# Kernel tuning notes

Measured on AMD Instinct MI355X. Metric: run time of the kernel, lower is better.

Reference implementation:

```python
import jax, jax.numpy as jnp
import numpy as np
import math

NQ = 8          # qubits
DIM = 2 ** NQ   # 256-dim state vector
NVL = 4         # variational layers
EPS = 1e-5      # LayerNorm eps (torch default)


def _ln(x, g, b):
    m = jnp.mean(x, -1, keepdims=True)
    v = jnp.mean((x - m) ** 2, -1, keepdims=True)
    return (x - m) / jnp.sqrt(v + EPS) * g + b


def _apply_ry(state, q, theta):
    # state: (B, 256); qubit q is the 2**q 'pre' axis (PennyLane wire 0 = MSB)
    pre, post = 2 ** q, 2 ** (NQ - 1 - q)
    s = state.reshape(-1, pre, 2, post)
    c = jnp.cos(theta * 0.5)
    sn = jnp.sin(theta * 0.5)
    if jnp.ndim(theta) == 1:  # per-sample angle (input encoding)
        c = c[:, None, None]
        sn = sn[:, None, None]
    a0 = s[:, :, 0, :]
    a1 = s[:, :, 1, :]
    return jnp.stack([c * a0 - sn * a1, sn * a0 + c * a1], axis=2).reshape(state.shape)


def _apply_cnot(state, ctrl):
    # CNOT with control=ctrl, target=ctrl+1 (adjacent wires)
    pre = 2 ** ctrl
    s = state.reshape(-1, pre, 2, 2, 2 ** (NQ - 2 - ctrl))
    new = jnp.stack([s[:, :, 0], s[:, :, 1, ::-1]], axis=2)
    return new.reshape(state.shape)


def _vqc(inputs, weights):
    # inputs: (B, 8), weights: (4, 8) -> (B, 8) PauliZ expectations
    B = inputs.shape[0]
    # Hadamard layer on |0...0> -> uniform real superposition, amp = 1/16
    state = jnp.full((B, DIM), 1.0 / 16.0, dtype=inputs.dtype)
    for q in range(NQ):
        state = _apply_ry(state, q, inputs[:, q])
    for l in range(NVL):
        for c in range(0, NQ - 1, 2):
            state = _apply_cnot(state, c)
        for c in range(1, NQ - 1, 2):
            state = _apply_cnot(state, c)
        for q in range(NQ):
            state = _apply_ry(state, q, weights[l, q])
    p = state * state  # state stays real (H, RY, CNOT are real gates)
    zs = []
    for q in range(NQ):
        pr = p.reshape(B, 2 ** q, 2, 2 ** (NQ - 1 - q))
        zs.append(pr[:, :, 0, :].sum((1, 2)) - pr[:, :, 1, :].sum((1, 2)))
    return jnp.stack(zs, axis=1)


def reference(x, pe, emb_w, emb_b, emb_g, emb_bt, ip_w, ip_b, in_g, in_b,
              wq_i, wq_f, wq_g, wq_o, pi_w, pi_b, pf_w, pf_b, pg_w, pg_b,
              po_w, po_b, on_g, on_b, out_w, out_b):
    B, T, _ = x.shape
    H = emb_w.shape[0]
    # embedding + LayerNorm (dropout = identity in eval) + positional encoding
    emb = _ln(x @ emb_w.T + emb_b, emb_g, emb_bt) + pe[None, :T]

    def step(carry, x_t):
        h, c = carry
        comb = jnp.concatenate([x_t, h], axis=1)
        proj = _ln(jnp.tanh(comb @ ip_w.T + ip_b), in_g, in_b)
        i_t = jax.nn.sigmoid(_vqc(proj, wq_i) @ pi_w.T + pi_b)
        f_t = jax.nn.sigmoid(_vqc(proj, wq_f) @ pf_w.T + pf_b)
        g_t = jnp.tanh(_vqc(proj, wq_g) @ pg_w.T + pg_b)
        o_t = jax.nn.sigmoid(_vqc(proj, wq_o) @ po_w.T + po_b)
        c_n = f_t * c + i_t * g_t
        h_n = o_t * jnp.tanh(c_n)
        out_t = _ln(h_n + x_t, on_g, on_b)
        return (h_n, c_n), out_t

    h0 = jnp.zeros((B, H), x.dtype)
    xs = jnp.swapaxes(emb, 0, 1)  # (T, B, H)
    _, outs = jax.lax.scan(jax.checkpoint(step), (h0, h0), xs)
    out = jnp.swapaxes(outs, 0, 1)  # (B, T, H)
    return out @ out_w.T + out_b


def setup_inputs() -> dict:
    B, T, IN, H, OUT = 1024, 128, 8, 128, 1
    key = jax.random.key(0)
    ks = jax.random.split(key, 12)

    def kaiming_u(k, shape, fan_in):
        bnd = math.sqrt(6.0 / fan_in)
        return jax.random.uniform(k, shape, jnp.float32, -bnd, bnd)

    # sinusoidal positional encoding
    pe = np.zeros((T, H), np.float32)
    pos = np.arange(T, dtype=np.float32)[:, None]
    div = np.exp(np.arange(0, H, 2, dtype=np.float32) * (-math.log(10000.0) / H))
    pe[:, 0::2] = np.sin(pos * div)
    pe[:, 1::2] = np.cos(pos * div)

    return {
        'x': jax.random.normal(ks[0], (B, T, IN), jnp.float32),
        'pe': jnp.asarray(pe),
        'emb_w': kaiming_u(ks[1], (H, IN), IN), 'emb_b': jnp.zeros((H,), jnp.float32),
        'emb_g': jnp.ones((H,), jnp.float32), 'emb_bt': jnp.zeros((H,), jnp.float32),
        'ip_w': kaiming_u(ks[2], (NQ, 2 * H), 2 * H), 'ip_b': jnp.zeros((NQ,), jnp.float32),
        'in_g': jnp.ones((NQ,), jnp.float32), 'in_b': jnp.zeros((NQ,), jnp.float32),
        'wq_i': 0.01 * jax.random.normal(ks[3], (NVL, NQ), jnp.float32),
        'wq_f': 0.01 * jax.random.normal(ks[4], (NVL, NQ), jnp.float32),
        'wq_g': 0.01 * jax.random.normal(ks[5], (NVL, NQ), jnp.float32),
        'wq_o': 0.01 * jax.random.normal(ks[6], (NVL, NQ), jnp.float32),
        'pi_w': kaiming_u(ks[7], (H, NQ), NQ), 'pi_b': jnp.zeros((H,), jnp.float32),
        'pf_w': kaiming_u(ks[8], (H, NQ), NQ), 'pf_b': jnp.zeros((H,), jnp.float32),
        'pg_w': kaiming_u(ks[9], (H, NQ), NQ), 'pg_b': jnp.zeros((H,), jnp.float32),
        'po_w': kaiming_u(ks[10], (H, NQ), NQ), 'po_b': jnp.zeros((H,), jnp.float32),
        'on_g': jnp.ones((H,), jnp.float32), 'on_b': jnp.zeros((H,), jnp.float32),
        'out_w': kaiming_u(ks[11], (OUT, H), H), 'out_b': jnp.zeros((OUT,), jnp.float32),
    }
```

## Files before the change

kernel.cpp:

```cpp
#include <hip/hip_runtime.h>

#define Tv 128

typedef float v2 __attribute__((ext_vector_type(2)));

__device__ __forceinline__ v2 pkfma(v2 a, v2 b, v2 c) {
  return __builtin_elementwise_fma(a, b, c);
}

template<int CTRL>
__device__ __forceinline__ float dppx(float x) {
  return __int_as_float(__builtin_amdgcn_update_dpp(0, __float_as_int(x), CTRL, 0xF, 0xF, true));
}
__device__ __forceinline__ float dpp_rm(float x, int ctrl, int rm) {
  switch (ctrl) {
    default: return 0.f;
    case 0x111: return __int_as_float(__builtin_amdgcn_update_dpp(0, __float_as_int(x), 0x111, 0xF, 0xF, true));
    case 0x112: return __int_as_float(__builtin_amdgcn_update_dpp(0, __float_as_int(x), 0x112, 0xF, 0xF, true));
    case 0x114: return __int_as_float(__builtin_amdgcn_update_dpp(0, __float_as_int(x), 0x114, 0xF, 0xF, true));
    case 0x118: return __int_as_float(__builtin_amdgcn_update_dpp(0, __float_as_int(x), 0x118, 0xF, 0xF, true));
    case 0x142: return __int_as_float(__builtin_amdgcn_update_dpp(0, __float_as_int(x), 0x142, 0xA, 0xF, true));
    case 0x143: return __int_as_float(__builtin_amdgcn_update_dpp(0, __float_as_int(x), 0x143, 0xC, 0xF, true));
  }
}
__device__ __forceinline__ float wave_sum(float x) {
  x += dpp_rm(x, 0x111, 0xF);
  x += dpp_rm(x, 0x112, 0xF);
  x += dpp_rm(x, 0x114, 0xF);
  x += dpp_rm(x, 0x118, 0xF);
  x += dpp_rm(x, 0x142, 0xA);
  x += dpp_rm(x, 0x143, 0xC);
  return __int_as_float(__builtin_amdgcn_readlane(__float_as_int(x), 63));
}
template<int M>
__device__ __forceinline__ float lane_xor(float x) {
  if constexpr (M == 1)       return dppx<0xB1>(x);
  else if constexpr (M == 2)  return dppx<0x4E>(x);
  else if constexpr (M == 8)  return dppx<0x128>(x);
  else if constexpr (M == 32) return __shfl_xor(x, 32, 64);
  else return __int_as_float(__builtin_amdgcn_ds_swizzle(__float_as_int(x), (M << 10) | 0x1F));
}
__device__ __forceinline__ float bperm(int addr, float x) {
  return __int_as_float(__builtin_amdgcn_ds_bpermute(addr, __float_as_int(x)));
}
__device__ __forceinline__ float rdlane(float x, int l) {
  return __int_as_float(__builtin_amdgcn_readlane(__float_as_int(x), l));
}
__device__ __forceinline__ float fast_rcp(float x){ return __builtin_amdgcn_rcpf(x); }
__device__ __forceinline__ float fast_rsq(float x){ return __builtin_amdgcn_rsqf(x); }
__device__ __forceinline__ float tanh_(float x){
  float e = __expf(2.0f * x);
  return 1.0f - 2.0f * fast_rcp(e + 1.0f);
}
__device__ __forceinline__ float sigm_(float x){
  return fast_rcp(1.0f + __expf(-x));
}

__device__ __forceinline__ float transpose_reduce8(const v2* P2, int L) {
  const int bb0 = L & 1, bb1 = L & 2, bb2 = L & 4;
  float q_[4];
  #pragma unroll
  for (int k = 0; k < 4; k++) {
    float keep = bb0 ? P2[k].y : P2[k].x;
    float send = bb0 ? P2[k].x : P2[k].y;
    q_[k] = keep + lane_xor<1>(send);
  }
  float r_[2];
  #pragma unroll
  for (int k = 0; k < 2; k++) {
    float keep = bb1 ? q_[2 * k + 1] : q_[2 * k];
    float send = bb1 ? q_[2 * k]     : q_[2 * k + 1];
    r_[k] = keep + lane_xor<2>(send);
  }
  float u;
  {
    float keep = bb2 ? r_[1] : r_[0];
    float send = bb2 ? r_[0] : r_[1];
    u = keep + lane_xor<4>(send);
  }
  u += lane_xor<8>(u); u += lane_xor<16>(u); u += lane_xor<32>(u);
  return u;
}

template<int M>
__device__ __forceinline__ void ry_lane_t(v2* S, float ts) {
  v2 ts2 = {ts, ts};
  #pragma unroll
  for (int k = 0; k < 4; k++) {
    v2 o;
    o.x = lane_xor<M>(S[k].x);
    o.y = lane_xor<M>(S[k].y);
    S[k] = pkfma(ts2, o, S[k]);
  }
}


struct __align__(16) SMem {
  float tt[4][36];
  float ipb[8][4];
  float zbuf[32];
  float embp[2][2];
  float projp[2][8];
  float outp[2][4];
};

__global__ __launch_bounds__(128, 2) void qlstm_kernel(
    const float* __restrict__ x,     const float* __restrict__ pe,
    const float* __restrict__ emb_w, const float* __restrict__ emb_b,
    const float* __restrict__ emb_g, const float* __restrict__ emb_bt,
    const float* __restrict__ ip_w,  const float* __restrict__ ip_b,
    const float* __restrict__ in_g,  const float* __restrict__ in_b,
    const float* __restrict__ wq_i,  const float* __restrict__ wq_f,
    const float* __restrict__ wq_gt, const float* __restrict__ wq_o,
    const float* __restrict__ pi_w,  const float* __restrict__ pi_b,
    const float* __restrict__ pf_w,  const float* __restrict__ pf_b,
    const float* __restrict__ pg_w,  const float* __restrict__ pg_b,
    const float* __restrict__ po_w,  const float* __restrict__ po_b,
    const float* __restrict__ on_g,  const float* __restrict__ on_b,
    const float* __restrict__ out_w, const float* __restrict__ out_b,
    float* __restrict__ out)
{
  __shared__ SMem sm;
  const int tid = threadIdx.x;
  const int b   = blockIdx.x;
  const int w   = tid >> 6;
  const int L   = tid & 63;
  const int l5  = L & 31;
  const int gate = w * 2 + (L >> 5);
  const int o8  = L & 7;

  {
    int gg = tid >> 5, rem = tid & 31;
    const float* wsel = (gg == 0) ? wq_i : (gg == 1) ? wq_f : (gg == 2) ? wq_gt : wq_o;
    float th = wsel[rem] * 0.5f;
    float cc = __cosf(th), ss = __sinf(th);
    sm.tt[gg][rem] = ss * fast_rcp(cc);
    float v = cc;
    v *= lane_xor<1>(v); v *= lane_xor<2>(v); v *= lane_xor<4>(v);
    v *= lane_xor<8>(v); v *= lane_xor<16>(v);
    if (rem == 0) sm.tt[gg][32] = v * v;
  }
  if (tid < 8) {
    sm.ipb[tid][0] = ip_b[tid];
    sm.ipb[tid][1] = in_g[tid];
    sm.ipb[tid][2] = in_b[tid];
    sm.ipb[tid][3] = 0.0f;
  }

  const int j = tid;
  v2 EW[4];
  {
    float4 a = *reinterpret_cast<const float4*>(emb_w + j * 8);
    float4 c = *reinterpret_cast<const float4*>(emb_w + j * 8 + 4);
    EW[0] = {a.x, a.y}; EW[1] = {a.z, a.w}; EW[2] = {c.x, c.y}; EW[3] = {c.z, c.w};
  }
  float ebb = emb_b[j], egg = emb_g[j], ebt = emb_bt[j];
  v2 IPW1[4], IPW2[4];
  #pragma unroll
  for (int k = 0; k < 4; k++) {
    IPW1[k] = {ip_w[(2 * k) * 256 + j],       ip_w[(2 * k + 1) * 256 + j]};
    IPW2[k] = {ip_w[(2 * k) * 256 + 128 + j], ip_w[(2 * k + 1) * 256 + 128 + j]};
  }
  v2 GW[4][4];
  #pragma unroll
  for (int gg = 0; gg < 4; gg++) {
    const float* pw = (gg == 0) ? pi_w : (gg == 1) ? pf_w : (gg == 2) ? pg_w : po_w;
    float4 a = *reinterpret_cast<const float4*>(pw + j * 8);
    float4 c = *reinterpret_cast<const float4*>(pw + j * 8 + 4);
    GW[gg][0] = {a.x, a.y}; GW[gg][1] = {a.z, a.w};
    GW[gg][2] = {c.x, c.y}; GW[gg][3] = {c.z, c.w};
  }
  float gb[4] = {pi_b[j], pf_b[j], pg_b[j], po_b[j]};
  float ong = on_g[j], onb = on_b[j], ow_ = out_w[j];
  float outb = out_b[0];
  float a_ = ong * ow_;

  const int grp = L & 32;
  int aC0, aC1;
  {
    int l1 = l5 ^ ((l5 & 16) >> 1) ^ ((l5 & 4) >> 1);
    int lb = l1 ^ ((l1 & 8) >> 1) ^ ((l1 & 2) >> 1);
    aC0 = (grp | lb) << 2;
    aC1 = (grp | (lb ^ 16)) << 2;
  }

  float h = 0.f, c = 0.f;
  const float* xbase = x + (size_t)b * Tv * 8;

  {
    float uw = transpose_reduce8(EW, L);
    float eb1 = wave_sum(ebb);
    if (L < 8) sm.projp[w][L] = uw;
    if (L == 0) sm.embp[w][0] = eb1;
  }
  __syncthreads();

  v2 WB[4]; float bS;
  {
    #pragma unroll
    for (int k = 0; k < 4; k++) {
      WB[k].x = (sm.projp[0][2 * k]     + sm.projp[1][2 * k])     * 0.0078125f;
      WB[k].y = (sm.projp[0][2 * k + 1] + sm.projp[1][2 * k + 1]) * 0.0078125f;
    }
    bS = (sm.embp[0][0] + sm.embp[1][0]) * 0.0078125f;
  }
  float4 ipbv = *reinterpret_cast<float4*>(&sm.ipb[o8][0]);
  v2 LT0[4], LT1[4], LNTS[4];
  float LTS[4][5];
  float ct2g = sm.tt[gate][32];
  {
    const float* tg = sm.tt[gate];
    #pragma unroll
    for (int l = 0; l < 4; l++) {
      float4 qa = *reinterpret_cast<const float4*>(tg + l * 8);
      float4 qb = *reinterpret_cast<const float4*>(tg + l * 8 + 4);
      LT0[l]  = {qa.x, qa.x};
      LT1[l]  = {qa.y, qa.y};
      LNTS[l] = {-qa.z, qa.z};
      float tq[5] = {qa.w, qb.x, qb.y, qb.z, qb.w};
      #pragma unroll
      for (int q = 0; q < 5; q++) {
        int m = 16 >> q;
        LTS[l][q] = (l5 & m) ? tq[q] : -tq[q];
      }
    }
  }

  float e;
  {
    float4 a = *reinterpret_cast<const float4*>(xbase);
    float4 cq = *reinterpret_cast<const float4*>(xbase + 4);
    v2 XT[4] = {{a.x,a.y},{a.z,a.w},{cq.x,cq.y},{cq.z,cq.w}};
    v2 acc = XT[0] * EW[0];
    acc = pkfma(XT[1], EW[1], acc);
    acc = pkfma(XT[2], EW[2], acc);
    acc = pkfma(XT[3], EW[3], acc);
    float er = ebb + acc.x + acc.y;
    float s2 = wave_sum(er * er);
    float r0 = wave_sum(a_), r1 = wave_sum(onb * ow_);
    if (L == 0) {
      sm.embp[w][1] = s2;
      sm.outp[w][0] = r0; sm.outp[w][1] = r1;
    }
    __syncthreads();
    v2 mac = XT[0] * WB[0];
    mac = pkfma(XT[1], WB[1], mac);
    mac = pkfma(XT[2], WB[2], mac);
    mac = pkfma(XT[3], WB[3], mac);
    float mn = mac.x + mac.y + bS;
    float s2t = sm.embp[0][1] + sm.embp[1][1];
    float vr = fmaf(s2t, 0.0078125f, -mn * mn);
    float inv = fast_rsq(vr + 1e-5f);
    e = (er - mn) * inv * egg + ebt + pe[j];
  }
  const float SW = sm.outp[0][0] + sm.outp[1][0];
  const float KB = sm.outp[0][1] + sm.outp[1][1] + outb;

  #pragma unroll 1
  for (int t = 0; t < Tv; t++) {
    v2 XN[4]; float pen;
    {
      int tn = (t + 1) & (Tv - 1);
      float4 a = *reinterpret_cast<const float4*>(xbase + tn * 8);
      float4 cq = *reinterpret_cast<const float4*>(xbase + tn * 8 + 4);
      XN[0] = {a.x,a.y}; XN[1] = {a.z,a.w}; XN[2] = {cq.x,cq.y}; XN[3] = {cq.z,cq.w};
      pen = pe[tn * 128 + j];
    }

    const v2 e2 = {e, e}, h2 = {h, h};
    v2 P2[4];
    #pragma unroll
    for (int k = 0; k < 4; k++)
      P2[k] = pkfma(e2, IPW1[k], h2 * IPW2[k]);
    float u = transpose_reduce8(P2, L);
    if (L < 8) sm.projp[w][L] = u;
    __syncthreads();
    u += sm.projp[1 - w][o8];
    if (t && tid == 0) {
      float sy  = sm.outp[0][0] + sm.outp[1][0];
      float sy2 = sm.outp[0][1] + sm.outp[1][1];
      float sya = sm.outp[0][2] + sm.outp[1][2];
      float mn2 = sy * 0.0078125f;
      float vr2 = fmaf(sy2, 0.0078125f, -mn2 * mn2);
      float inv2 = fast_rsq(vr2 + 1e-5f);
      out[b * Tv + t - 1] = fmaf(inv2, sya - mn2 * SW, KB);
    }

    float tv = tanh_(u + ipbv.x);
    float m1 = tv, m2 = tv * tv;
    m1 += lane_xor<1>(m1); m2 += lane_xor<1>(m2);
    m1 += lane_xor<2>(m1); m2 += lane_xor<2>(m2);
    m1 += lane_xor<4>(m1); m2 += lane_xor<4>(m2);
    float pm = m1 * 0.125f;
    float pv = fmaf(m2, 0.125f, -pm * pm);
    float theta = (tv - pm) * fast_rsq(pv + 1e-5f) * ipbv.y + ipbv.z;
    float ph = theta * 0.5f;
    float cE = __cosf(ph), sE = __sinf(ph);
    float fm = cE - sE, fp = cE + sE;
    float f_[16];
    #pragma unroll
    for (int qq = 0; qq < 8; qq++) {
      f_[2 * qq]     = rdlane(fm, qq);
      f_[2 * qq + 1] = rdlane(fp, qq);
    }

    v2 S[4];
    {
      float g01_[4];
      #pragma unroll
      for (int i = 0; i < 4; i++)
        g01_[i] = f_[(i >> 1) & 1] * f_[2 + (i & 1)];
      float lf = f_[6 + ((l5 >> 4) & 1)] * f_[8 + ((l5 >> 3) & 1)]
               * f_[10 + ((l5 >> 2) & 1)] * f_[12 + ((l5 >> 1) & 1)]
               * f_[14 + (l5 & 1)];
      lf *= 0.0625f;
      const v2 F45 = {f_[4], f_[5]};
      #pragma unroll
      for (int k = 0; k < 4; k++) {
        float tk = lf * g01_[k];
        v2 tk2 = {tk, tk};
        S[k] = tk2 * F45;
      }
    }

    #pragma unroll
    for (int l = 0; l < 4; l++) {
      v2 N0, N1, N2, N3;
      N0.x = bperm(aC0, S[0].x); N0.y = bperm(aC1, S[0].y);
      N1.x = bperm(aC1, S[1].y); N1.y = bperm(aC0, S[1].x);
      N2.x = bperm(aC0, S[3].x); N2.y = bperm(aC1, S[3].y);
      N3.x = bperm(aC1, S[2].y); N3.y = bperm(aC0, S[2].x);
      S[0] = N0; S[1] = N1; S[2] = N2; S[3] = N3;
      {
        v2 t0 = LT0[l];
        v2 a0 = S[0], a1 = S[1];
        S[0] = pkfma(-t0, S[2], S[0]);
        S[2] = pkfma( t0, a0,  S[2]);
        S[1] = pkfma(-t0, S[3], S[1]);
        S[3] = pkfma( t0, a1,  S[3]);
      }
      {
        v2 t1 = LT1[l];
        v2 a0 = S[0], a2 = S[2];
        S[0] = pkfma(-t1, S[1], S[0]);
        S[1] = pkfma( t1, a0,  S[1]);
        S[2] = pkfma(-t1, S[3], S[2]);
        S[3] = pkfma( t1, a2,  S[3]);
      }
      {
        v2 nts = LNTS[l];
        #pragma unroll
        for (int k = 0; k < 4; k++) {
          v2 aa = S[k];
          v2 sw = __builtin_shufflevector(aa, aa, 1, 0);
          S[k] = pkfma(nts, sw, aa);
        }
      }
      ry_lane_t<16>(S, LTS[l][0]);
      ry_lane_t<8>(S, LTS[l][1]);
      ry_lane_t<4>(S, LTS[l][2]);
      ry_lane_t<2>(S, LTS[l][3]);
      ry_lane_t<1>(S, LTS[l][4]);
    }

    v2 P[4];
    #pragma unroll
    for (int k = 0; k < 4; k++) P[k] = S[k] * S[k];
    v2 A = P[0] + P[2];
    v2 B = P[1] + P[3];
    v2 D = (P[0] - P[2]) + (P[1] - P[3]);
    float z0 = D.x + D.y;
    v2 Ev = A - B;
    float z1 = Ev.x + Ev.y;
    v2 G = A + B;
    float z2 = G.x - G.y;
    float S_ = G.x + G.y;
    z0 += lane_xor<1>(z0); z1 += lane_xor<1>(z1); z2 += lane_xor<1>(z2);
    z0 += lane_xor<2>(z0); z1 += lane_xor<2>(z1); z2 += lane_xor<2>(z2);
    z0 += lane_xor<4>(z0); z1 += lane_xor<4>(z1); z2 += lane_xor<4>(z2);
    z0 += lane_xor<8>(z0); z1 += lane_xor<8>(z1); z2 += lane_xor<8>(z2);
    z0 += lane_xor<16>(z0); z1 += lane_xor<16>(z1); z2 += lane_xor<16>(z2);
    float v, d, uS;
    v = lane_xor<16>(S_); d = S_ - v; uS = S_ + v;
    float z3 = (l5 & 16) ? -d : d;
    z3 += lane_xor<8>(z3); z3 += lane_xor<4>(z3); z3 += lane_xor<2>(z3); z3 += lane_xor<1>(z3);
    v = lane_xor<8>(uS); d = uS - v; uS = uS + v;
    float z4 = (l5 & 8) ? -d : d;
    z4 += lane_xor<4>(z4); z4 += lane_xor<2>(z4); z4 += lane_xor<1>(z4);
    v = lane_xor<4>(uS); d = uS - v; uS = uS + v;
    float z5 = (l5 & 4) ? -d : d;
    z5 += lane_xor<2>(z5); z5 += lane_xor<1>(z5);
    v = lane_xor<2>(uS); d = uS - v; uS = uS + v;
    float z6 = (l5 & 2) ? -d : d;
    z6 += lane_xor<1>(z6);
    v = lane_xor<1>(uS); d = uS - v;
    float z7 = (l5 & 1) ? -d : d;

    if (l5 < 8) {
      float zv = z0;
      zv = (l5 == 1) ? z1 : zv;
      zv = (l5 == 2) ? z2 : zv;
      zv = (l5 == 3) ? z3 : zv;
      zv = (l5 == 4) ? z4 : zv;
      zv = (l5 == 5) ? z5 : zv;
      zv = (l5 == 6) ? z6 : zv;
      zv = (l5 == 7) ? z7 : zv;
      sm.zbuf[gate * 8 + l5] = zv * ct2g;
    }

    v2 acc = XN[0] * EW[0];
    acc = pkfma(XN[1], EW[1], acc);
    acc = pkfma(XN[2], EW[2], acc);
    acc = pkfma(XN[3], EW[3], acc);
    float en_raw = ebb + acc.x + acc.y;
    {
      float s2n = wave_sum(en_raw * en_raw);
      if (L == 0) sm.embp[w][0] = s2n;
    }
    __syncthreads();

    float acg[4];
    #pragma unroll
    for (int gg = 0; gg < 4; gg++) {
      float4 za0 = *reinterpret_cast<float4*>(&sm.zbuf[gg * 8]);
      float4 za1 = *reinterpret_cast<float4*>(&sm.zbuf[gg * 8 + 4]);
      v2 Z0 = {za0.x, za0.y}, Z1 = {za0.z, za0.w};
      v2 Z2 = {za1.x, za1.y}, Z3 = {za1.z, za1.w};
      v2 av = Z0 * GW[gg][0];
      av = pkfma(Z1, GW[gg][1], av);
      av = pkfma(Z2, GW[gg][2], av);
      av = pkfma(Z3, GW[gg][3], av);
      acg[gg] = gb[gg] + av.x + av.y;
    }
    float it = sigm_(acg[0]), ft = sigm_(acg[1]), gt = tanh_(acg[2]), ot = sigm_(acg[3]);
    c = ft * c + it * gt;
    h = ot * tanh_(c);

    float en;
    {
      float s2 = sm.embp[0][0] + sm.embp[1][0];
      v2 mac = XN[0] * WB[0];
      mac = pkfma(XN[1], WB[1], mac);
      mac = pkfma(XN[2], WB[2], mac);
      mac = pkfma(XN[3], WB[3], mac);
      float mn = mac.x + mac.y + bS;
      float vr = fmaf(s2, 0.0078125f, -mn * mn);
      float inv = fast_rsq(vr + 1e-5f);
      en = (en_raw - mn) * inv * egg + ebt + pen;
    }

    {
      float y = h + e;
      float ry0 = wave_sum(y), ry1 = wave_sum(y * y), ry2 = wave_sum(y * a_);
      if (L == 0) { sm.outp[w][0] = ry0; sm.outp[w][1] = ry1; sm.outp[w][2] = ry2; }
    }
    e = en;
  }

  __syncthreads();
  if (tid == 0) {
    float sy  = sm.outp[0][0] + sm.outp[1][0];
    float sy2 = sm.outp[0][1] + sm.outp[1][1];
    float sya = sm.outp[0][2] + sm.outp[1][2];
    float mn2 = sy * 0.0078125f;
    float vr2 = fmaf(sy2, 0.0078125f, -mn2 * mn2);
    float inv2 = fast_rsq(vr2 + 1e-5f);
    out[b * Tv + Tv - 1] = fmaf(inv2, sya - mn2 * SW, KB);
  }
}

extern "C" void kernel_launch(void* const* d_in, const int* in_sizes, int n_in,
                              void* d_out, int out_size, void* d_ws, size_t ws_size,
                              hipStream_t stream) {
  qlstm_kernel<<<dim3(1024), dim3(128), 0, stream>>>(
      (const float*)d_in[0],  (const float*)d_in[1],  (const float*)d_in[2],  (const float*)d_in[3],
      (const float*)d_in[4],  (const float*)d_in[5],  (const float*)d_in[6],  (const float*)d_in[7],
      (const float*)d_in[8],  (const float*)d_in[9],  (const float*)d_in[10], (const float*)d_in[11],
      (const float*)d_in[12], (const float*)d_in[13], (const float*)d_in[14], (const float*)d_in[15],
      (const float*)d_in[16], (const float*)d_in[17], (const float*)d_in[18], (const float*)d_in[19],
      (const float*)d_in[20], (const float*)d_in[21], (const float*)d_in[22], (const float*)d_in[23],
      (const float*)d_in[24], (const float*)d_in[25],
      (float*)d_out);
}
```

Baseline: 549.7 us.

## Process two batch sequences per block to interleave independent recurrences

Each block now runs two independent batch elements (b and b+512) through the recurrent loop together, halving the grid to 512 blocks. Work for both sequences is interleaved between the same barriers, so the per-step __syncthreads and shuffle latency is shared and there is more independent work to hide latency. The cost is higher register pressure: launch bounds drop to one block per SIMD group, so occupancy may fall and spilling is possible.

```diff
diff --git a/kernel.cpp b/kernel.cpp
--- a/kernel.cpp
+++ b/kernel.cpp
@@ -1,6 +1,7 @@
 #include <hip/hip_runtime.h>
 
 #define Tv 128
+#define BH 512
 
 typedef float v2 __attribute__((ext_vector_type(2)));
 
@@ -98,13 +99,13 @@
 struct __align__(16) SMem {
   float tt[4][36];
   float ipb[8][4];
-  float zbuf[32];
-  float embp[2][2];
-  float projp[2][8];
-  float outp[2][4];
+  float zbuf[2][32];
+  float embp[2][2][2];
+  float projp[2][2][8];
+  float outp[2][2][4];
 };
 
-__global__ __launch_bounds__(128, 2) void qlstm_kernel(
+__global__ __launch_bounds__(128, 1) void qlstm_kernel(
     const float* __restrict__ x,     const float* __restrict__ pe,
     const float* __restrict__ emb_w, const float* __restrict__ emb_b,
     const float* __restrict__ emb_g, const float* __restrict__ emb_bt,
@@ -184,14 +185,14 @@
     aC1 = (grp | (lb ^ 16)) << 2;
   }
 
-  float h = 0.f, c = 0.f;
-  const float* xbase = x + (size_t)b * Tv * 8;
+  float h[2] = {0.f, 0.f}, c[2] = {0.f, 0.f};
+  const float* xb[2] = { x + (size_t)b * Tv * 8, x + (size_t)(b + BH) * Tv * 8 };
 
   {
     float uw = transpose_reduce8(EW, L);
     float eb1 = wave_sum(ebb);
-    if (L < 8) sm.projp[w][L] = uw;
-    if (L == 0) sm.embp[w][0] = eb1;
+    if (L < 8) sm.projp[0][w][L] = uw;
+    if (L == 0) sm.embp[0][w][0] = eb1;
   }
   __syncthreads();
 
@@ -199,10 +200,10 @@
   {
     #pragma unroll
     for (int k = 0; k < 4; k++) {
-      WB[k].x = (sm.projp[0][2 * k]     + sm.projp[1][2 * k])     * 0.0078125f;
-      WB[k].y = (sm.projp[0][2 * k + 1] + sm.projp[1][2 * k + 1]) * 0.0078125f;
-    }
-    bS = (sm.embp[0][0] + sm.embp[1][0]) * 0.0078125f;
+      WB[k].x = (sm.projp[0][0][2 * k]     + sm.projp[0][1][2 * k])     * 0.0078125f;
+      WB[k].y = (sm.projp[0][0][2 * k + 1] + sm.projp[0][1][2 * k + 1]) * 0.0078125f;
+    }
+    bS = (sm.embp[0][0][0] + sm.embp[0][1][0]) * 0.0078125f;
   }
   float4 ipbv = *reinterpret_cast<float4*>(&sm.ipb[o8][0]);
   v2 LT0[4], LT1[4], LNTS[4];
@@ -226,86 +227,104 @@
     }
   }
 
-  float e;
-  {
-    float4 a = *reinterpret_cast<const float4*>(xbase);
-    float4 cq = *reinterpret_cast<const float4*>(xbase + 4);
-    v2 XT[4] = {{a.x,a.y},{a.z,a.w},{cq.x,cq.y},{cq.z,cq.w}};
-    v2 acc = XT[0] * EW[0];
-    acc = pkfma(XT[1], EW[1], acc);
-    acc = pkfma(XT[2], EW[2], acc);
-    acc = pkfma(XT[3], EW[3], acc);
-    float er = ebb + acc.x + acc.y;
-    float s2 = wave_sum(er * er);
+  float e[2];
+  {
+    v2 XT[2][4]; float er[2];
+    #pragma unroll
+    for (int ee = 0; ee < 2; ee++) {
+      float4 a = *reinterpret_cast<const float4*>(xb[ee]);
+      float4 cq = *reinterpret_cast<const float4*>(xb[ee] + 4);
+      XT[ee][0] = {a.x,a.y}; XT[ee][1] = {a.z,a.w};
+      XT[ee][2] = {cq.x,cq.y}; XT[ee][3] = {cq.z,cq.w};
+      v2 acc = XT[ee][0] * EW[0];
+      acc = pkfma(XT[ee][1], EW[1], acc);
+      acc = pkfma(XT[ee][2], EW[2], acc);
+      acc = pkfma(XT[ee][3], EW[3], acc);
+      er[ee] = ebb + acc.x + acc.y;
+      float s2 = wave_sum(er[ee] * er[ee]);
+      if (L == 0) sm.embp[ee][w][1] = s2;
+    }
     float r0 = wave_sum(a_), r1 = wave_sum(onb * ow_);
-    if (L == 0) {
-      sm.embp[w][1] = s2;
-      sm.outp[w][0] = r0; sm.outp[w][1] = r1;
-    }
+    if (L == 0) { sm.outp[0][w][0] = r0; sm.outp[0][w][1] = r1; }
     __syncthreads();
-    v2 mac = XT[0] * WB[0];
-    mac = pkfma(XT[1], WB[1], mac);
-    mac = pkfma(XT[2], WB[2], mac);
-    mac = pkfma(XT[3], WB[3], mac);
-    float mn = mac.x + mac.y + bS;
-    float s2t = sm.embp[0][1] + sm.embp[1][1];
-    float vr = fmaf(s2t, 0.0078125f, -mn * mn);
-    float inv = fast_rsq(vr + 1e-5f);
-    e = (er - mn) * inv * egg + ebt + pe[j];
-  }
-  const float SW = sm.outp[0][0] + sm.outp[1][0];
-  const float KB = sm.outp[0][1] + sm.outp[1][1] + outb;
+    #pragma unroll
+    for (int ee = 0; ee < 2; ee++) {
+      v2 mac = XT[ee][0] * WB[0];
+      mac = pkfma(XT[ee][1], WB[1], mac);
+      mac = pkfma(XT[ee][2], WB[2], mac);
+      mac = pkfma(XT[ee][3], WB[3], mac);
+      float mn = mac.x + mac.y + bS;
+      float s2t = sm.embp[ee][0][1] + sm.embp[ee][1][1];
+      float vr = fmaf(s2t, 0.0078125f, -mn * mn);
+      float inv = fast_rsq(vr + 1e-5f);
+      e[ee] = (er[ee] - mn) * inv * egg + ebt + pe[j];
+    }
+  }
+  const float SW = sm.outp[0][0][0] + sm.outp[0][1][0];
+  const float KB = sm.outp[0][0][1] + sm.outp[0][1][1] + outb;
 
   #pragma unroll 1
   for (int t = 0; t < Tv; t++) {
-    v2 XN[4]; float pen;
+    v2 XN[2][4]; float pen;
     {
       int tn = (t + 1) & (Tv - 1);
-      float4 a = *reinterpret_cast<const float4*>(xbase + tn * 8);
-      float4 cq = *reinterpret_cast<const float4*>(xbase + tn * 8 + 4);
-      XN[0] = {a.x,a.y}; XN[1] = {a.z,a.w}; XN[2] = {cq.x,cq.y}; XN[3] = {cq.z,cq.w};
+      #pragma unroll
+      for (int ee = 0; ee < 2; ee++) {
+        float4 a = *reinterpret_cast<const float4*>(xb[ee] + tn * 8);
+        float4 cq = *reinterpret_cast<const float4*>(xb[ee] + tn * 8 + 4);
+        XN[ee][0] = {a.x,a.y}; XN[ee][1] = {a.z,a.w};
+        XN[ee][2] = {cq.x,cq.y}; XN[ee][3] = {cq.z,cq.w};
+      }
       pen = pe[tn * 128 + j];
     }
 
-    const v2 e2 = {e, e}, h2 = {h, h};
-    v2 P2[4];
-    #pragma unroll
-    for (int k = 0; k < 4; k++)
-      P2[k] = pkfma(e2, IPW1[k], h2 * IPW2[k]);
-    float u = transpose_reduce8(P2, L);
-    if (L < 8) sm.projp[w][L] = u;
+    float u[2];
+    #pragma unroll
+    for (int ee = 0; ee < 2; ee++) {
+      const v2 e2 = {e[ee], e[ee]}, h2 = {h[ee], h[ee]};
+      v2 P2[4];
+      #pragma unroll
+      for (int k = 0; k < 4; k++)
+        P2[k] = pkfma(e2, IPW1[k], h2 * IPW2[k]);
+      u[ee] = transpose_reduce8(P2, L);
+      if (L < 8) sm.projp[ee][w][L] = u[ee];
+    }
     __syncthreads();
-    u += sm.projp[1 - w][o8];
+    u[0] += sm.projp[0][1 - w][o8];
+    u[1] += sm.projp[1][1 - w][o8];
     if (t && tid == 0) {
-      float sy  = sm.outp[0][0] + sm.outp[1][0];
-      float sy2 = sm.outp[0][1] + sm.outp[1][1];
-      float sya = sm.outp[0][2] + sm.outp[1][2];
-      float mn2 = sy * 0.0078125f;
-      float vr2 = fmaf(sy2, 0.0078125f, -mn2 * mn2);
-      float inv2 = fast_rsq(vr2 + 1e-5f);
-      out[b * Tv + t - 1] = fmaf(inv2, sya - mn2 * SW, KB);
-    }
-
-    float tv = tanh_(u + ipbv.x);
-    float m1 = tv, m2 = tv * tv;
-    m1 += lane_xor<1>(m1); m2 += lane_xor<1>(m2);
-    m1 += lane_xor<2>(m1); m2 += lane_xor<2>(m2);
-    m1 += lane_xor<4>(m1); m2 += lane_xor<4>(m2);
-    float pm = m1 * 0.125f;
-    float pv = fmaf(m2, 0.125f, -pm * pm);
-    float theta = (tv - pm) * fast_rsq(pv + 1e-5f) * ipbv.y + ipbv.z;
-    float ph = theta * 0.5f;
-    float cE = __cosf(ph), sE = __sinf(ph);
-    float fm = cE - sE, fp = cE + sE;
-    float f_[16];
-    #pragma unroll
-    for (int qq = 0; qq < 8; qq++) {
-      f_[2 * qq]     = rdlane(fm, qq);
-      f_[2 * qq + 1] = rdlane(fp, qq);
-    }
-
-    v2 S[4];
-    {
+      #pragma unroll
+      for (int ee = 0; ee < 2; ee++) {
+        float sy  = sm.outp[ee][0][0] + sm.outp[ee][1][0];
+        float sy2 = sm.outp[ee][0][1] + sm.outp[ee][1][1];
+        float sya = sm.outp[ee][0][2] + sm.outp[ee][1][2];
+        float mn2 = sy * 0.0078125f;
+        float vr2 = fmaf(sy2, 0.0078125f, -mn2 * mn2);
+        float inv2 = fast_rsq(vr2 + 1e-5f);
+        out[(size_t)(b + ee * BH) * Tv + t - 1] = fmaf(inv2, sya - mn2 * SW, KB);
+      }
+    }
+
+    v2 S[2][4];
+    #pragma unroll
+    for (int ee = 0; ee < 2; ee++) {
+      float tv = tanh_(u[ee] + ipbv.x);
+      float m1 = tv, m2 = tv * tv;
+      m1 += lane_xor<1>(m1); m2 += lane_xor<1>(m2);
+      m1 += lane_xor<2>(m1); m2 += lane_xor<2>(m2);
+      m1 += lane_xor<4>(m1); m2 += lane_xor<4>(m2);
+      float pm = m1 * 0.125f;
+      float pv = fmaf(m2, 0.125f, -pm * pm);
+      float theta = (tv - pm) * fast_rsq(pv + 1e-5f) * ipbv.y + ipbv.z;
+      float ph = theta * 0.5f;
+      float cE = __cosf(ph), sE = __sinf(ph);
+      float fm = cE - sE, fp = cE + sE;
+      float f_[16];
+      #pragma unroll
+      for (int qq = 0; qq < 8; qq++) {
+        f_[2 * qq]     = rdlane(fm, qq);
+        f_[2 * qq + 1] = rdlane(fp, qq);
+      }
       float g01_[4];
       #pragma unroll
       for (int i = 0; i < 4; i++)
@@ -319,160 +338,172 @@
       for (int k = 0; k < 4; k++) {
         float tk = lf * g01_[k];
         v2 tk2 = {tk, tk};
-        S[k] = tk2 * F45;
+        S[ee][k] = tk2 * F45;
       }
     }
 
     #pragma unroll
     for (int l = 0; l < 4; l++) {
-      v2 N0, N1, N2, N3;
-      N0.x = bperm(aC0, S[0].x); N0.y = bperm(aC1, S[0].y);
-      N1.x = bperm(aC1, S[1].y); N1.y = bperm(aC0, S[1].x);
-      N2.x = bperm(aC0, S[3].x); N2.y = bperm(aC1, S[3].y);
-      N3.x = bperm(aC1, S[2].y); N3.y = bperm(aC0, S[2].x);
-      S[0] = N0; S[1] = N1; S[2] = N2; S[3] = N3;
-      {
-        v2 t0 = LT0[l];
-        v2 a0 = S[0], a1 = S[1];
-        S[0] = pkfma(-t0, S[2], S[0]);
-        S[2] = pkfma( t0, a0,  S[2]);
-        S[1] = pkfma(-t0, S[3], S[1]);
-        S[3] = pkfma( t0, a1,  S[3]);
-      }
-      {
-        v2 t1 = LT1[l];
-        v2 a0 = S[0], a2 = S[2];
-        S[0] = pkfma(-t1, S[1], S[0]);
-        S[1] = pkfma( t1, a0,  S[1]);
-        S[2] = pkfma(-t1, S[3], S[2]);
-        S[3] = pkfma( t1, a2,  S[3]);
-      }
-      {
-        v2 nts = LNTS[l];
-        #pragma unroll
-        for (int k = 0; k < 4; k++) {
-          v2 aa = S[k];
-          v2 sw = __builtin_shufflevector(aa, aa, 1, 0);
-          S[k] = pkfma(nts, sw, aa);
+      #pragma unroll
+      for (int ee = 0; ee < 2; ee++) {
+        v2* Se = S[ee];
+        v2 N0, N1, N2, N3;
+        N0.x = bperm(aC0, Se[0].x); N0.y = bperm(aC1, Se[0].y);
+        N1.x = bperm(aC1, Se[1].y); N1.y = bperm(aC0, Se[1].x);
+        N2.x = bperm(aC0, Se[3].x); N2.y = bperm(aC1, Se[3].y);
+        N3.x = bperm(aC1, Se[2].y); N3.y = bperm(aC0, Se[2].x);
+        Se[0] = N0; Se[1] = N1; Se[2] = N2; Se[3] = N3;
+        {
+          v2 t0 = LT0[l];
+          v2 a0 = Se[0], a1 = Se[1];
+          Se[0] = pkfma(-t0, Se[2], Se[0]);
+          Se[2] = pkfma( t0, a0,  Se[2]);
+          Se[1] = pkfma(-t0, Se[3], Se[1]);
+          Se[3] = pkfma( t0, a1,  Se[3]);
         }
-      }
-      ry_lane_t<16>(S, LTS[l][0]);
-      ry_lane_t<8>(S, LTS[l][1]);
-      ry_lane_t<4>(S, LTS[l][2]);
-      ry_lane_t<2>(S, LTS[l][3]);
-      ry_lane_t<1>(S, LTS[l][4]);
-    }
-
-    v2 P[4];
-    #pragma unroll
-    for (int k = 0; k < 4; k++) P[k] = S[k] * S[k];
-    v2 A = P[0] + P[2];
-    v2 B = P[1] + P[3];
-    v2 D = (P[0] - P[2]) + (P[1] - P[3]);
-    float z0 = D.x + D.y;
-    v2 Ev = A - B;
-    float z1 = Ev.x + Ev.y;
-    v2 G = A + B;
-    float z2 = G.x - G.y;
-    float S_ = G.x + G.y;
-    z0 += lane_xor<1>(z0); z1 += lane_xor<1>(z1); z2 += lane_xor<1>(z2);
-    z0 += lane_xor<2>(z0); z1 += lane_xor<2>(z1); z2 += lane_xor<2>(z2);
-    z0 += lane_xor<4>(z0); z1 += lane_xor<4>(z1); z2 += lane_xor<4>(z2);
-    z0 += lane_xor<8>(z0); z1 += lane_xor<8>(z1); z2 += lane_xor<8>(z2);
-    z0 += lane_xor<16>(z0); z1 += lane_xor<16>(z1); z2 += lane_xor<16>(z2);
-    float v, d, uS;
-    v = lane_xor<16>(S_); d = S_ - v; uS = S_ + v;
-    float z3 = (l5 & 16) ? -d : d;
-    z3 += lane_xor<8>(z3); z3 += lane_xor<4>(z3); z3 += lane_xor<2>(z3); z3 += lane_xor<1>(z3);
-    v = lane_xor<8>(uS); d = uS - v; uS = uS + v;
-    float z4 = (l5 & 8) ? -d : d;
-    z4 += lane_xor<4>(z4); z4 += lane_xor<2>(z4); z4 += lane_xor<1>(z4);
-    v = lane_xor<4>(uS); d = uS - v; uS = uS + v;
-    float z5 = (l5 & 4) ? -d : d;
-    z5 += lane_xor<2>(z5); z5 += lane_xor<1>(z5);
-    v = lane_xor<2>(uS); d = uS - v; uS = uS + v;
-    float z6 = (l5 & 2) ? -d : d;
-    z6 += lane_xor<1>(z6);
-    v = lane_xor<1>(uS); d = uS - v;
-    float z7 = (l5 & 1) ? -d : d;
-
-    if (l5 < 8) {
-      float zv = z0;
-      zv = (l5 == 1) ? z1 : zv;
-      zv = (l5 == 2) ? z2 : zv;
-      zv = (l5 == 3) ? z3 : zv;
-      zv = (l5 == 4) ? z4 : zv;
-      zv = (l5 == 5) ? z5 : zv;
-      zv = (l5 == 6) ? z6 : zv;
-      zv = (l5 == 7) ? z7 : zv;
-      sm.zbuf[gate * 8 + l5] = zv * ct2g;
-    }
-
-    v2 acc = XN[0] * EW[0];
-    acc = pkfma(XN[1], EW[1], acc);
-    acc = pkfma(XN[2], EW[2], acc);
-    acc = pkfma(XN[3], EW[3], acc);
-    float en_raw = ebb + acc.x + acc.y;
-    {
-      float s2n = wave_sum(en_raw * en_raw);
-      if (L == 0) sm.embp[w][0] = s2n;
+        {
+          v2 t1 = LT1[l];
+          v2 a0 = Se[0], a2 = Se[2];
+          Se[0] = pkfma(-t1, Se[1], Se[0]);
+          Se[1] = pkfma( t1, a0,  Se[1]);
+          Se[2] = pkfma(-t1, Se[3], Se[2]);
+          Se[3] = pkfma( t1, a2,  Se[3]);
+        }
+        {
+          v2 nts = LNTS[l];
+          #pragma unroll
+          for (int k = 0; k < 4; k++) {
+            v2 aa = Se[k];
+            v2 sw = __builtin_shufflevector(aa, aa, 1, 0);
+            Se[k] = pkfma(nts, sw, aa);
+          }
+        }
+        ry_lane_t<16>(Se, LTS[l][0]);
+        ry_lane_t<8>(Se, LTS[l][1]);
+        ry_lane_t<4>(Se, LTS[l][2]);
+        ry_lane_t<2>(Se, LTS[l][3]);
+        ry_lane_t<1>(Se, LTS[l][4]);
+      }
+    }
+
+    #pragma unroll
+    for (int ee = 0; ee < 2; ee++) {
+      v2 P[4];
+      #pragma unroll
+      for (int k = 0; k < 4; k++) P[k] = S[ee][k] * S[ee][k];
+      v2 A = P[0] + P[2];
+      v2 B = P[1] + P[3];
+      v2 D = (P[0] - P[2]) + (P[1] - P[3]);
+      float z0 = D.x + D.y;
+      v2 Ev = A - B;
+      float z1 = Ev.x + Ev.y;
+      v2 G = A + B;
+      float z2 = G.x - G.y;
+      float S_ = G.x + G.y;
+      z0 += lane_xor<1>(z0); z1 += lane_xor<1>(z1); z2 += lane_xor<1>(z2);
+      z0 += lane_xor<2>(z0); z1 += lane_xor<2>(z1); z2 += lane_xor<2>(z2);
+      z0 += lane_xor<4>(z0); z1 += lane_xor<4>(z1); z2 += lane_xor<4>(z2);
+      z0 += lane_xor<8>(z0); z1 += lane_xor<8>(z1); z2 += lane_xor<8>(z2);
+      z0 += lane_xor<16>(z0); z1 += lane_xor<16>(z1); z2 += lane_xor<16>(z2);
+      float v, d, uS;
+      v = lane_xor<16>(S_); d = S_ - v; uS = S_ + v;
+      float z3 = (l5 & 16) ? -d : d;
+      z3 += lane_xor<8>(z3); z3 += lane_xor<4>(z3); z3 += lane_xor<2>(z3); z3 += lane_xor<1>(z3);
+      v = lane_xor<8>(uS); d = uS - v; uS = uS + v;
+      float z4 = (l5 & 8) ? -d : d;
+      z4 += lane_xor<4>(z4); z4 += lane_xor<2>(z4); z4 += lane_xor<1>(z4);
+      v = lane_xor<4>(uS); d = uS - v; uS = uS + v;
+      float z5 = (l5 & 4) ? -d : d;
+      z5 += lane_xor<2>(z5); z5 += lane_xor<1>(z5);
+      v = lane_xor<2>(uS); d = uS - v; uS = uS + v;
+      float z6 = (l5 & 2) ? -d : d;
+      z6 += lane_xor<1>(z6);
+      v = lane_xor<1>(uS); d = uS - v;
+      float z7 = (l5 & 1) ? -d : d;
+
+      if (l5 < 8) {
+        float zv = z0;
+        zv = (l5 == 1) ? z1 : zv;
+        zv = (l5 == 2) ? z2 : zv;
+        zv = (l5 == 3) ? z3 : zv;
+        zv = (l5 == 4) ? z4 : zv;
+        zv = (l5 == 5) ? z5 : zv;
+        zv = (l5 == 6) ? z6 : zv;
+        zv = (l5 == 7) ? z7 : zv;
+        sm.zbuf[ee][gate * 8 + l5] = zv * ct2g;
+      }
+    }
+
+    float en_raw[2];
+    #pragma unroll
+    for (int ee = 0; ee < 2; ee++) {
+      v2 acc = XN[ee][0] * EW[0];
+      acc = pkfma(XN[ee][1], EW[1], acc);
+      acc = pkfma(XN[ee][2], EW[2], acc);
+      acc = pkfma(XN[ee][3], EW[3], acc);
+      en_raw[ee] = ebb + acc.x + acc.y;
+      float s2n = wave_sum(en_raw[ee] * en_raw[ee]);
+      if (L == 0) sm.embp[ee][w][0] = s2n;
     }
     __syncthreads();
 
-    float acg[4];
-    #pragma unroll
-    for (int gg = 0; gg < 4; gg++) {
-      float4 za0 = *reinterpret_cast<float4*>(&sm.zbuf[gg * 8]);
-      float4 za1 = *reinterpret_cast<float4*>(&sm.zbuf[gg * 8 + 4]);
-      v2 Z0 = {za0.x, za0.y}, Z1 = {za0.z, za0.w};
-      v2 Z2 = {za1.x, za1.y}, Z3 = {za1.z, za1.w};
-      v2 av = Z0 * GW[gg][0];
-      av = pkfma(Z1, GW[gg][1], av);
-      av = pkfma(Z2, GW[gg][2], av);
-      av = pkfma(Z3, GW[gg][3], av);
-      acg[gg] = gb[gg] + av.x + av.y;
-    }
-    float it = sigm_(acg[0]), ft = sigm_(acg[1]), gt = tanh_(acg[2]), ot = sigm_(acg[3]);
-    c = ft * c + it * gt;
-    h = ot * tanh_(c);
-
-    float en;
-    {
-      float s2 = sm.embp[0][0] + sm.embp[1][0];
-      v2 mac = XN[0] * WB[0];
-      mac = pkfma(XN[1], WB[1], mac);
-      mac = pkfma(XN[2], WB[2], mac);
-      mac = pkfma(XN[3], WB[3], mac);
+    #pragma unroll
+    for (int ee = 0; ee < 2; ee++) {
+      float acg[4];
+      #pragma unroll
+      for (int gg = 0; gg < 4; gg++) {
+        float4 za0 = *reinterpret_cast<float4*>(&sm.zbuf[ee][gg * 8]);
+        float4 za1 = *reinterpret_cast<float4*>(&sm.zbuf[ee][gg * 8 + 4]);
+        v2 Z0 = {za0.x, za0.y}, Z1 = {za0.z, za0.w};
+        v2 Z2 = {za1.x, za1.y}, Z3 = {za1.z, za1.w};
+        v2 av = Z0 * GW[gg][0];
+        av = pkfma(Z1, GW[gg][1], av);
+        av = pkfma(Z2, GW[gg][2], av);
+        av = pkfma(Z3, GW[gg][3], av);
+        acg[gg] = gb[gg] + av.x + av.y;
+      }
+      float it = sigm_(acg[0]), ft = sigm_(acg[1]), gt = tanh_(acg[2]), ot = sigm_(acg[3]);
+      c[ee] = ft * c[ee] + it * gt;
+      h[ee] = ot * tanh_(c[ee]);
+    }
+
+    #pragma unroll
+    for (int ee = 0; ee < 2; ee++) {
+      float s2 = sm.embp[ee][0][0] + sm.embp[ee][1][0];
+      v2 mac = XN[ee][0] * WB[0];
+      mac = pkfma(XN[ee][1], WB[1], mac);
+      mac = pkfma(XN[ee][2], WB[2], mac);
+      mac = pkfma(XN[ee][3], WB[3], mac);
       float mn = mac.x + mac.y + bS;
       float vr = fmaf(s2, 0.0078125f, -mn * mn);
       float inv = fast_rsq(vr + 1e-5f);
-      en = (en_raw - mn) * inv * egg + ebt + pen;
-    }
-
-    {
-      float y = h + e;
+      float en = (en_raw[ee] - mn) * inv * egg + ebt + pen;
+      float y = h[ee] + e[ee];
       float ry0 = wave_sum(y), ry1 = wave_sum(y * y), ry2 = wave_sum(y * a_);
-      if (L == 0) { sm.outp[w][0] = ry0; sm.outp[w][1] = ry1; sm.outp[w][2] = ry2; }
-    }
-    e = en;
+      if (L == 0) { sm.outp[ee][w][0] = ry0; sm.outp[ee][w][1] = ry1; sm.outp[ee][w][2] = ry2; }
+      e[ee] = en;
+    }
   }
 
   __syncthreads();
   if (tid == 0) {
-    float sy  = sm.outp[0][0] + sm.outp[1][0];
-    float sy2 = sm.outp[0][1] + sm.outp[1][1];
-    float sya = sm.outp[0][2] + sm.outp[1][2];
-    float mn2 = sy * 0.0078125f;
-    float vr2 = fmaf(sy2, 0.0078125f, -mn2 * mn2);
-    float inv2 = fast_rsq(vr2 + 1e-5f);
-    out[b * Tv + Tv - 1] = fmaf(inv2, sya - mn2 * SW, KB);
+    #pragma unroll
+    for (int ee = 0; ee < 2; ee++) {
+      float sy  = sm.outp[ee][0][0] + sm.outp[ee][1][0];
+      float sy2 = sm.outp[ee][0][1] + sm.outp[ee][1][1];
+      float sya = sm.outp[ee][0][2] + sm.outp[ee][1][2];
+      float mn2 = sy * 0.0078125f;
+      float vr2 = fmaf(sy2, 0.0078125f, -mn2 * mn2);
+      float inv2 = fast_rsq(vr2 + 1e-5f);
+      out[(size_t)(b + ee * BH) * Tv + Tv - 1] = fmaf(inv2, sya - mn2 * SW, KB);
+    }
   }
 }
 
 extern "C" void kernel_launch(void* const* d_in, const int* in_sizes, int n_in,
                               void* d_out, int out_size, void* d_ws, size_t ws_size,
                               hipStream_t stream) {
-  qlstm_kernel<<<dim3(1024), dim3(128), 0, stream>>>(
+  qlstm_kernel<<<dim3(BH), dim3(128), 0, stream>>>(
       (const float*)d_in[0],  (const float*)d_in[1],  (const float*)d_in[2],  (const float*)d_in[3],
       (const float*)d_in[4],  (const float*)d_in[5],  (const float*)d_in[6],  (const float*)d_in[7],
       (const float*)d_in[8],  (const float*)d_in[9],  (const float*)d_in[10], (const float*)d_in[11],
```

Measured after the change: 1.004 ms. 82.7% more time.
